# Kernel optimization log

Hardware: AMD Instinct MI355X
Metric: run time of the kernel (lower is better)

The kernel has to match this reference:

```python
import math
import jax, jax.numpy as jnp
import numpy as np

HEADS = 16
DIM_HEAD = 64
BSZ = 16        # block_size
EPS = 1e-8


def _flip_every_two(t):
    # t: (B, nblk, z, d) -> flip adjacent pairs along nblk
    B, nblk = t.shape[0], t.shape[1]
    t = t.reshape(B, nblk // 2, 2, *t.shape[2:])
    t = jnp.flip(t, axis=2)
    return t.reshape(B, nblk, *t.shape[3:])


def setup_inputs() -> dict:
    key = jax.random.key(0)
    k1, k2, k3 = jax.random.split(key, 3)
    b, n, dim = 4, 8192, 1024
    inner = HEADS * DIM_HEAD
    x = jax.random.normal(k1, (b, n, dim), dtype=jnp.float32)
    w_qkv = jax.random.normal(k2, (dim, inner * 3), dtype=jnp.float32) * 0.02
    w_out = jax.random.normal(k3, (inner, dim), dtype=jnp.float32) * 0.02
    b_out = jnp.zeros((dim,), dtype=jnp.float32)
    return {"x": x, "w_qkv": w_qkv, "w_out": w_out, "b_out": b_out}


def _hattention(x, w_qkv, w_out, b_out):
    b, n, dim = x.shape  # n assumed power of 2 -> no padding needed
    scale = DIM_HEAD ** -0.5

    qkv = x @ w_qkv                                   # (b, n, 3*inner)
    q, k, v = jnp.split(qkv, 3, axis=-1)

    def to_heads(t):
        return t.reshape(b, n, HEADS, DIM_HEAD).transpose(0, 2, 1, 3).reshape(b * HEADS, n, DIM_HEAD)

    q, k, v = map(to_heads, (q, k, v))
    q = q * scale

    num_levels = int(math.log2(n // BSZ)) - 1

    # build coarsened pyramid: q,k averaged over pairs, v summed
    qkvs = [(q, k, v)]
    for _ in range(num_levels):
        B, m, d = q.shape
        q = q.reshape(B, m // 2, 2, d).mean(axis=2)
        k = k.reshape(B, m // 2, 2, d).mean(axis=2)
        v = v.reshape(B, m // 2, 2, d).sum(axis=2)
        qkvs.append((q, k, v))

    def to_blocks(t):
        return t.reshape(t.shape[0], -1, BSZ, DIM_HEAD)

    Ys = []
    L = len(qkvs)
    for ind, (ql, kl, vl) in enumerate(reversed(qkvs)):
        is_last = ind == L - 1
        qb, kb, vb = map(to_blocks, (ql, kl, vl))
        if not is_last:
            kb = _flip_every_two(kb)
            vb = _flip_every_two(vb)
        # block-local unnormalized softmax attention
        S = jnp.einsum('bnid,bnjd->bnij', qb, kb)
        S = S - jnp.max(S, axis=-1, keepdims=True)
        A = jnp.exp(S)
        y = jnp.einsum('bnij,bnjd->bnid', A, vb)
        Asum = A.sum(axis=-1)
        Ys.append((y.reshape(y.shape[0], -1, DIM_HEAD),
                   Asum.reshape(Asum.shape[0], -1)))

    # combine coarse-to-fine by upsampling (repeat by 2) and summing
    Y, A = Ys[0]
    for Yl, Al in Ys[1:]:
        Y = jnp.repeat(Y, 2, axis=1) + Yl
        A = jnp.repeat(A, 2, axis=1) + Al

    out = Y / (A + EPS)[..., None]                    # (b*h, n, d)
    out = out.reshape(b, HEADS, n, DIM_HEAD).transpose(0, 2, 1, 3).reshape(b, n, HEADS * DIM_HEAD)
    return out @ w_out + b_out


def reference(x, w_qkv, w_out, b_out):
    return _hattention(x, w_qkv, w_out, b_out)
```

## Files before the change

### kernel.cpp

```cpp
#include <hip/hip_runtime.h>
#include <hip/hip_bf16.h>

typedef __bf16 bf16_t;
typedef bf16_t bf16x8 __attribute__((ext_vector_type(8)));
typedef float f32x4 __attribute__((ext_vector_type(4)));

#define PROWS 16352

__device__ __forceinline__ void gl_lds16(const bf16_t* g, bf16_t* l) {
  __builtin_amdgcn_global_load_lds(
      (const __attribute__((address_space(1))) void*)g,
      (__attribute__((address_space(3))) void*)l,
      16, 0, 0);
}

__device__ __forceinline__ void load8f(const bf16_t* p, float* f) {
  bf16x8 v = *(const bf16x8*)p;
#pragma unroll
  for (int e = 0; e < 8; ++e) f[e] = (float)v[e];
}
__device__ __forceinline__ void store8f(bf16_t* p, const float* f) {
  bf16x8 v;
#pragma unroll
  for (int e = 0; e < 8; ++e) v[e] = (bf16_t)f[e];
  *(bf16x8*)p = v;
}

__global__ __launch_bounds__(256) void cvt_f32_to_bf16(const float* __restrict__ in,
                                                       bf16_t* __restrict__ o) {
  size_t gid = (size_t)blockIdx.x * 256 + threadIdx.x;
  const float4* p = (const float4*)in + gid * 2;
  float4 a = p[0], b = p[1];
  bf16x8 v;
  v[0] = (bf16_t)a.x; v[1] = (bf16_t)a.y; v[2] = (bf16_t)a.z; v[3] = (bf16_t)a.w;
  v[4] = (bf16_t)b.x; v[5] = (bf16_t)b.y; v[6] = (bf16_t)b.z; v[7] = (bf16_t)b.w;
  *(bf16x8*)(o + gid * 8) = v;
}

__global__ __launch_bounds__(256) void transpose_to_bf16(const float* __restrict__ w,
                                                         bf16_t* __restrict__ wT,
                                                         int K, int N) {
  __shared__ float t[32][33];
  int bx = blockIdx.x, by = blockIdx.y;
  int tx = threadIdx.x & 31, ty = threadIdx.x >> 5;
#pragma unroll
  for (int r = ty; r < 32; r += 8)
    t[r][tx] = w[(size_t)(by * 32 + r) * N + bx * 32 + tx];
  __syncthreads();
#pragma unroll
  for (int r = ty; r < 32; r += 8)
    wT[(size_t)(bx * 32 + r) * K + by * 32 + tx] = (bf16_t)t[tx][r];
}

template <int EPI>
__global__ __launch_bounds__(512, 2) void gemm256p(const bf16_t* __restrict__ A,
                                                   const bf16_t* __restrict__ Bt,
                                                   float* __restrict__ Cp,
                                                   const float* __restrict__ bias,
                                                   bf16_t* __restrict__ Pq,
                                                   bf16_t* __restrict__ Pk,
                                                   bf16_t* __restrict__ Pv,
                                                   int ldc, int nTilesN, int tilesPerBlock) {
  __shared__ __align__(16) bf16_t As[2 * 256 * 64];
  __shared__ __align__(16) bf16_t Bs[2 * 256 * 64];
  const int LD = 1024;
  const int tid = threadIdx.x;
  const int w = tid >> 6, lane = tid & 63;

  const int chunk = (blockIdx.x & 7) * 32 + (blockIdx.x >> 3);
  const int tile0 = chunk * tilesPerBlock;
  const int nSteps = tilesPerBlock * 16;

  const int wr = w >> 2, wc = w & 3;
  const int lr = lane & 15, lg = lane >> 4;
  const int sw = lr & 7;
  f32x4 acc[8][4] = {};

  auto stageHalf = [&](const bf16_t* __restrict__ G, int rbase, int kt,
                       bf16_t* lbuf, int h) {
#pragma unroll
    for (int j = 0; j < 2; ++j) {
      int b = j * 8 + w;
      int r3 = lane >> 3;
      int k8 = (lane & 7) ^ r3;
      gl_lds16(G + (size_t)(rbase + h * 128 + b * 8 + r3) * LD + kt + k8 * 8,
               lbuf + h * 8192 + b * 512);
    }
  };

  int ntEc = tile0 % nTilesN;
  int bmE = (tile0 / nTilesN) * 256, bnE = ntEc * 256;
  int nt2c = ntEc, bm2 = bmE, bn2 = bnE, kt2 = 128;

  stageHalf(Bt, bnE, 0, Bs, 0); stageHalf(Bt, bnE, 0, Bs, 1);
  stageHalf(A, bmE, 0, As, 0);  stageHalf(A, bmE, 0, As, 1);
  stageHalf(Bt, bnE, 64, Bs + 16384, 0); stageHalf(Bt, bnE, 64, Bs + 16384, 1);
  stageHalf(A, bmE, 64, As + 16384, 0);  stageHalf(A, bmE, 64, As + 16384, 1);
  asm volatile("s_waitcnt vmcnt(8)" ::: "memory");
  __syncthreads();

  for (int g = 0; g < nSteps; ++g) {
    const int c = g & 1;
    bf16_t* Abuf = As + c * 16384;
    bf16_t* Bbuf = Bs + c * 16384;
    const bool pf = (g + 2) < nSteps;
    bf16x8 bfrag[4][2];

#pragma unroll
    for (int p = 0; p < 4; ++p) {
      bf16x8 afrag[2][2];
#pragma unroll
      for (int fi = 0; fi < 2; ++fi)
#pragma unroll
        for (int kk = 0; kk < 2; ++kk)
          afrag[fi][kk] = *(const bf16x8*)&Abuf[(wr * 128 + p * 32 + fi * 16 + lr) * 64 +
                                                (((kk * 4 + lg) ^ sw) * 8)];
      if (p == 0) {
#pragma unroll
        for (int fj = 0; fj < 4; ++fj)
#pragma unroll
          for (int kk = 0; kk < 2; ++kk)
            bfrag[fj][kk] = *(const bf16x8*)&Bbuf[(wc * 64 + fj * 16 + lr) * 64 +
                                                  (((kk * 4 + lg) ^ sw) * 8)];
      }
      if (pf) {
        if (p == 1) stageHalf(Bt, bn2, kt2, Bbuf, 0);
        if (p == 2) stageHalf(Bt, bn2, kt2, Bbuf, 1);
        if (p == 3) { stageHalf(A, bm2, kt2, Abuf, 0); stageHalf(A, bm2, kt2, Abuf, 1); }
      }
      __builtin_amdgcn_s_barrier();
      asm volatile("s_waitcnt lgkmcnt(0)" ::: "memory");
      __builtin_amdgcn_sched_barrier(0);
      __builtin_amdgcn_s_setprio(1);
#pragma unroll
      for (int kk = 0; kk < 2; ++kk)
#pragma unroll
        for (int fi = 0; fi < 2; ++fi)
#pragma unroll
          for (int fj = 0; fj < 4; ++fj)
            acc[p * 2 + fi][fj] = __builtin_amdgcn_mfma_f32_16x16x32_bf16(
                afrag[fi][kk], bfrag[fj][kk], acc[p * 2 + fi][fj], 0, 0, 0);
      __builtin_amdgcn_s_setprio(0);
      if (p == 3) {
        if (pf) asm volatile("s_waitcnt vmcnt(8)" ::: "memory");
        else    asm volatile("s_waitcnt vmcnt(0)" ::: "memory");
      }
      __builtin_amdgcn_s_barrier();
    }

    kt2 += 64;
    if (kt2 == 1024) {
      kt2 = 0; ++nt2c; bn2 += 256;
      if (nt2c == nTilesN) { nt2c = 0; bn2 = 0; bm2 += 256; }
    }

    if ((g & 15) == 15) {
      if (EPI == 1) {
        float bv[4];
#pragma unroll
        for (int fj = 0; fj < 4; ++fj) bv[fj] = bias[bnE + wc * 64 + fj * 16 + lr];
#pragma unroll
        for (int fi = 0; fi < 8; ++fi)
#pragma unroll
          for (int fj = 0; fj < 4; ++fj)
#pragma unroll
            for (int r = 0; r < 4; ++r) {
              int row = bmE + wr * 128 + fi * 16 + lg * 4 + r;
              int col = bnE + wc * 64 + fj * 16 + lr;
              Cp[(size_t)row * ldc + col] = acc[fi][fj][r] + bv[fj];
            }
      } else {
        const int trow0 = (bmE & 8191) + wr * 128 + lg * 4;
        const int hgRow = (bmE >> 13) << 4;
#pragma unroll
        for (int fj = 0; fj < 4; ++fj) {
          int col = bnE + wc * 64 + fj * 16 + lr;
          int tns = col >> 10, col10 = col & 1023;
          int h = col10 >> 6, d = col10 & 63;
          bf16_t* Pt = (tns == 0) ? Pq : (tns == 1 ? Pk : Pv);
          bf16_t* bp = Pt + ((size_t)(hgRow + h) * PROWS + trow0) * 64 + d;
          float scl = (tns == 0) ? 0.125f : 1.f;
#pragma unroll
          for (int fi = 0; fi < 8; ++fi)
#pragma unroll
            for (int r = 0; r < 4; ++r)
              bp[(fi * 16 + r) * 64] = (bf16_t)(acc[fi][fj][r] * scl);
        }
      }
#pragma unroll
      for (int fi = 0; fi < 8; ++fi)
#pragma unroll
        for (int fj = 0; fj < 4; ++fj) acc[fi][fj] = (f32x4){};
      ++ntEc; bnE += 256;
      if (ntEc == nTilesN) { ntEc = 0; bnE = 0; bmE += 256; }
    }
  }
}

__global__ __launch_bounds__(512) void coarsen_tree(bf16_t* __restrict__ Pq,
                                                    bf16_t* __restrict__ Pk,
                                                    bf16_t* __restrict__ Pv) {
  __shared__ float l6s[8][64];
  const int poffA[9] = {0, 8192, 12288, 14336, 15360, 15872, 16128, 16256, 16320};
  const int hg = blockIdx.x >> 4, win = blockIdx.x & 15;
  const int tid = threadIdx.x;
  const int d8 = tid & 7;
  const int tb = tid >> 3;
  const int wv = tid >> 6;
  const size_t base = (size_t)hg * PROWS;
  const int r0 = win * 512 + tb * 8;

#pragma unroll 1
  for (int tensor = 0; tensor < 3; ++tensor) {
    bf16_t* P = (tensor == 0) ? Pq : (tensor == 1 ? Pk : Pv);
    const float sc = (tensor == 2) ? 1.f : 0.5f;
    float v[8][8];
#pragma unroll
    for (int i = 0; i < 8; ++i) load8f(P + (base + r0 + i) * 64 + d8 * 8, v[i]);
    float a1[4][8];
#pragma unroll
    for (int i = 0; i < 4; ++i) {
#pragma unroll
      for (int e = 0; e < 8; ++e) a1[i][e] = sc * (v[2 * i][e] + v[2 * i + 1][e]);
      store8f(P + (base + poffA[1] + win * 256 + tb * 4 + i) * 64 + d8 * 8, a1[i]);
    }
    float a2[2][8];
#pragma unroll
    for (int i = 0; i < 2; ++i) {
#pragma unroll
      for (int e = 0; e < 8; ++e) a2[i][e] = sc * (a1[2 * i][e] + a1[2 * i + 1][e]);
      store8f(P + (base + poffA[2] + win * 128 + tb * 2 + i) * 64 + d8 * 8, a2[i]);
    }
    float a3[8];
#pragma unroll
    for (int e = 0; e < 8; ++e) a3[e] = sc * (a2[0][e] + a2[1][e]);
    store8f(P + (base + poffA[3] + win * 64 + tb) * 64 + d8 * 8, a3);
    float a4[8];
#pragma unroll
    for (int e = 0; e < 8; ++e) a4[e] = sc * (a3[e] + __shfl_xor(a3[e], 8, 64));
    if ((tb & 1) == 0) store8f(P + (base + poffA[4] + win * 32 + (tb >> 1)) * 64 + d8 * 8, a4);
    float a5[8];
#pragma unroll
    for (int e = 0; e < 8; ++e) a5[e] = sc * (a4[e] + __shfl_xor(a4[e], 16, 64));
    if ((tb & 3) == 0) store8f(P + (base + poffA[5] + win * 16 + (tb >> 2)) * 64 + d8 * 8, a5);
    float a6[8];
#pragma unroll
    for (int e = 0; e < 8; ++e) a6[e] = sc * (a5[e] + __shfl_xor(a5[e], 32, 64));
    if ((tb & 7) == 0) {
      bf16x8 o;
#pragma unroll
      for (int e = 0; e < 8; ++e) { l6s[wv][d8 * 8 + e] = a6[e]; o[e] = (bf16_t)a6[e]; }
      *(bf16x8*)(P + (base + poffA[6] + win * 8 + wv) * 64 + d8 * 8) = o;
    }
    __syncthreads();
    if (tid < 32) {
      int pr = tid >> 3;
      float a7[8];
#pragma unroll
      for (int e = 0; e < 8; ++e)
        a7[e] = sc * (l6s[2 * pr][d8 * 8 + e] + l6s[2 * pr + 1][d8 * 8 + e]);
      store8f(P + (base + poffA[7] + win * 4 + pr) * 64 + d8 * 8, a7);
      if (pr < 2) {
        float a8[8];
#pragma unroll
        for (int e = 0; e < 8; ++e)
          a8[e] = sc * (sc * (l6s[4 * pr][d8 * 8 + e] + l6s[4 * pr + 1][d8 * 8 + e]) +
                        sc * (l6s[4 * pr + 2][d8 * 8 + e] + l6s[4 * pr + 3][d8 * 8 + e]));
        store8f(P + (base + poffA[8] + win * 2 + pr) * 64 + d8 * 8, a8);
      }
    }
    __syncthreads();
  }
}


__global__ __launch_bounds__(256) void attn_hi(bf16_t* __restrict__ Pq,
                                               const bf16_t* __restrict__ Pk,
                                               const bf16_t* __restrict__ Pv,
                                               float* __restrict__ Asum) {
  const int poffA[9] = {0, 8192, 12288, 14336, 15360, 15872, 16128, 16256, 16320};
  const int tid = threadIdx.x;
  const int wv = tid >> 6, lane = tid & 63;
  const int lr = lane & 15, lg = lane >> 4;

  int bid = blockIdx.x * 4 + wv;
  int l = 4, cnt = 2048;
  while (bid >= cnt) { bid -= cnt; cnt >>= 1; ++l; }
  const int lg2nblk = 9 - l;
  const int blk = bid & ((1 << lg2nblk) - 1);
  const int hg = bid >> lg2nblk;
  const int kvblk = blk ^ 1;
  const size_t qbase = (size_t)hg * PROWS + poffA[l] + blk * 16;
  const size_t kvbase = (size_t)hg * PROWS + poffA[l] + kvblk * 16;

  f32x4 s = {};
#pragma unroll
  for (int c = 0; c < 2; ++c) {
    bf16x8 ak = *(const bf16x8*)(Pk + (kvbase + lr) * 64 + c * 32 + lg * 8);
    bf16x8 bq = *(const bf16x8*)(Pq + (qbase + lr) * 64 + c * 32 + lg * 8);
    s = __builtin_amdgcn_mfma_f32_16x16x32_bf16(ak, bq, s, 0, 0, 0);
  }
  float mx = fmaxf(fmaxf(s[0], s[1]), fmaxf(s[2], s[3]));
  mx = fmaxf(mx, __shfl_xor(mx, 16, 64));
  mx = fmaxf(mx, __shfl_xor(mx, 32, 64));
  float a[4]; float asum = 0.f;
#pragma unroll
  for (int r = 0; r < 4; ++r) { a[r] = (float)(bf16_t)__expf(s[r] - mx); asum += a[r]; }
  asum += __shfl_xor(asum, 16, 64);
  asum += __shfl_xor(asum, 32, 64);
  if (lg == 0) Asum[qbase + lr] = asum;

  const int src0 = (2 * lg) * 16 + lr;
  const int src1 = (2 * lg + 1) * 16 + lr;
  bf16x8 pa;
#pragma unroll
  for (int r = 0; r < 4; ++r) {
    float c0 = __shfl(a[r], src0, 64);
    float c1 = __shfl(a[r], src1, 64);
    pa[r]     = (lg < 2) ? (bf16_t)c0 : (bf16_t)0.f;
    pa[r + 4] = (lg < 2) ? (bf16_t)c1 : (bf16_t)0.f;
  }
#pragma unroll
  for (int dt = 0; dt < 4; ++dt) {
    bf16x8 vf;
    if (lg < 2) {
#pragma unroll
      for (int e = 0; e < 8; ++e) vf[e] = Pv[(kvbase + lg * 8 + e) * 64 + dt * 16 + lr];
    } else {
#pragma unroll
      for (int e = 0; e < 8; ++e) vf[e] = (bf16_t)0.f;
    }
    f32x4 y = __builtin_amdgcn_mfma_f32_16x16x32_bf16(pa, vf, (f32x4){}, 0, 0, 0);
#pragma unroll
    for (int r = 0; r < 4; ++r)
      Pq[(qbase + 4 * lg + r) * 64 + dt * 16 + lr] = (bf16_t)y[r];
  }
}

__global__ __launch_bounds__(256) void attn_comb(const bf16_t* __restrict__ Pq,
                                                 const bf16_t* __restrict__ Pk,
                                                 const bf16_t* __restrict__ Pv,
                                                 const float* __restrict__ Ab,
                                                 bf16_t* __restrict__ attnb) {
  __shared__ __align__(16) bf16_t yl[480 * 72];
  __shared__ float asl[480];
  const int poffA[9] = {0, 8192, 12288, 14336, 15360, 15872, 16128, 16256, 16320};
  const int loffA[4] = {0, 256, 384, 448};
  const int hg = blockIdx.x >> 5, win = blockIdx.x & 31;
  const int tid = threadIdx.x;
  const int wv = tid >> 6, lane = tid & 63;
  const int lr = lane & 15, lg = lane >> 4;

  auto do_attn = [&](int l, int blkL) {
    const int nb = 16 >> l;
    const int blk = win * nb + blkL;
    const int kvblk = l ? (blk ^ 1) : blk;
    const size_t qbase = (size_t)hg * PROWS + poffA[l] + (size_t)blk * 16;
    const size_t kvbase = (size_t)hg * PROWS + poffA[l] + (size_t)kvblk * 16;
    const int lrow = loffA[l] + blkL * 16;

    f32x4 s = {};
#pragma unroll
    for (int c = 0; c < 2; ++c) {
      bf16x8 ak = *(const bf16x8*)(Pk + (kvbase + lr) * 64 + c * 32 + lg * 8);
      bf16x8 bq = *(const bf16x8*)(Pq + (qbase + lr) * 64 + c * 32 + lg * 8);
      s = __builtin_amdgcn_mfma_f32_16x16x32_bf16(ak, bq, s, 0, 0, 0);
    }
    float mx = fmaxf(fmaxf(s[0], s[1]), fmaxf(s[2], s[3]));
    mx = fmaxf(mx, __shfl_xor(mx, 16, 64));
    mx = fmaxf(mx, __shfl_xor(mx, 32, 64));
    float a[4]; float asum = 0.f;
#pragma unroll
    for (int r = 0; r < 4; ++r) { a[r] = (float)(bf16_t)__expf(s[r] - mx); asum += a[r]; }
    asum += __shfl_xor(asum, 16, 64);
    asum += __shfl_xor(asum, 32, 64);
    if (lg == 0) asl[lrow + lr] = asum;

    const int src0 = (2 * lg) * 16 + lr;
    const int src1 = (2 * lg + 1) * 16 + lr;
    bf16x8 pa;
#pragma unroll
    for (int r = 0; r < 4; ++r) {
      float c0 = __shfl(a[r], src0, 64);
      float c1 = __shfl(a[r], src1, 64);
      pa[r]     = (lg < 2) ? (bf16_t)c0 : (bf16_t)0.f;
      pa[r + 4] = (lg < 2) ? (bf16_t)c1 : (bf16_t)0.f;
    }
#pragma unroll
    for (int dt = 0; dt < 4; ++dt) {
      bf16x8 vf;
      if (lg < 2) {
#pragma unroll
        for (int e = 0; e < 8; ++e) vf[e] = Pv[(kvbase + lg * 8 + e) * 64 + dt * 16 + lr];
      } else {
#pragma unroll
        for (int e = 0; e < 8; ++e) vf[e] = (bf16_t)0.f;
      }
      f32x4 y = __builtin_amdgcn_mfma_f32_16x16x32_bf16(pa, vf, (f32x4){}, 0, 0, 0);
#pragma unroll
      for (int r = 0; r < 4; ++r)
        yl[(lrow + 4 * lg + r) * 72 + dt * 16 + lr] = (bf16_t)y[r];
    }
  };

  do_attn(0, wv * 4 + 0); do_attn(0, wv * 4 + 1);
  do_attn(0, wv * 4 + 2); do_attn(0, wv * 4 + 3);
  do_attn(1, wv * 2 + 0); do_attn(1, wv * 2 + 1);
  do_attn(2, wv);
  if (wv < 2) do_attn(3, wv);
  __syncthreads();

  const int d8 = tid & 7, rg = tid >> 3;
#pragma unroll
  for (int i = 0; i < 8; ++i) {
    const int r = rg * 8 + i;
    const int t = win * 256 + r;
    float acc[8] = {};
    float asum = 0.f;
#pragma unroll
    for (int l = 0; l < 4; ++l) {
      const int row = loffA[l] + (r >> l);
      asum += asl[row];
      bf16x8 v = *(const bf16x8*)&yl[row * 72 + d8 * 8];
#pragma unroll
      for (int e = 0; e < 8; ++e) acc[e] += (float)v[e];
    }
#pragma unroll
    for (int l = 4; l < 9; ++l) {
      const size_t grow = (size_t)hg * PROWS + poffA[l] + (t >> l);
      asum += Ab[grow];
      bf16x8 v = *(const bf16x8*)(Pq + grow * 64 + d8 * 8);
#pragma unroll
      for (int e = 0; e < 8; ++e) acc[e] += (float)v[e];
    }
    const float inv = 1.f / (asum + 1e-8f);
    bf16x8 o;
#pragma unroll
    for (int e = 0; e < 8; ++e) o[e] = (bf16_t)(acc[e] * inv);
    *(bf16x8*)(attnb + ((size_t)(hg >> 4) * 8192 + t) * 1024 + (hg & 15) * 64 + d8 * 8) = o;
  }
}

extern "C" void kernel_launch(void* const* d_in, const int* in_sizes, int n_in,
                              void* d_out, int out_size, void* d_ws, size_t ws_size,
                              hipStream_t stream) {
  const float* x = (const float*)d_in[0];
  const float* wqkv = (const float*)d_in[1];
  const float* wout = (const float*)d_in[2];
  const float* bout = (const float*)d_in[3];
  float* out = (float*)d_out;
  (void)in_sizes; (void)n_in; (void)out_size; (void)ws_size;

  char* base = (char*)d_ws;
  bf16_t* Pq    = (bf16_t*)(base + 0);
  bf16_t* Pk    = (bf16_t*)(base + 133955584);
  bf16_t* Pv    = (bf16_t*)(base + 267911168);
  float*  Ab    = (float*)(base + 401866752);
  bf16_t* woutT = (bf16_t*)(base + 406052864);
  bf16_t* x_bf  = (bf16_t*)(base + 408150016);
  bf16_t* wqkvT = (bf16_t*)(base + 475258880);
  bf16_t* attnb = (bf16_t*)(base + 408150016);

  cvt_f32_to_bf16<<<16384, 256, 0, stream>>>(x, x_bf);
  transpose_to_bf16<<<dim3(96, 32), 256, 0, stream>>>(wqkv, wqkvT, 1024, 3072);
  transpose_to_bf16<<<dim3(32, 32), 256, 0, stream>>>(wout, woutT, 1024, 1024);

  gemm256p<0><<<256, 512, 0, stream>>>(x_bf, wqkvT, nullptr, nullptr, Pq, Pk, Pv,
                                       3072, 12, 6);

  coarsen_tree<<<1024, 512, 0, stream>>>(Pq, Pk, Pv);

  attn_hi<<<992, 256, 0, stream>>>(Pq, Pk, Pv, Ab);
  attn_comb<<<2048, 256, 0, stream>>>(Pq, Pk, Pv, Ab, attnb);

  gemm256p<1><<<256, 512, 0, stream>>>(attnb, woutT, out, bout, nullptr, nullptr, nullptr,
                                       1024, 4, 2);
}
```

Baseline: 592.7 us.

## Skip storing pyramid levels 1-3; recompute coarse q/k/v on the fly in attn_comb

The coarsening kernel no longer writes levels 1-3 of the q/k/v pyramid. It sums 8 rows directly and emits only levels 4-8, with finer-grained blocks (256 threads, 2048 blocks). attn_comb recomputes coarse q and k for levels 1-3 by averaging 2^l fine rows on the fly. It handles coarse v by spreading the attention weights across the fine rows and running several MFMA chunks. This removes a large amount of global writes and reads of intermediate levels, in exchange for more loads and MFMAs in attn_comb and slightly different bf16 rounding of the coarse levels.

```diff
diff --git a/kernel.cpp b/kernel.cpp
--- a/kernel.cpp
+++ b/kernel.cpp
@@ -197,82 +197,73 @@
   }
 }
 
-__global__ __launch_bounds__(512) void coarsen_tree(bf16_t* __restrict__ Pq,
+__global__ __launch_bounds__(256) void coarsen_lite(bf16_t* __restrict__ Pq,
                                                     bf16_t* __restrict__ Pk,
                                                     bf16_t* __restrict__ Pv) {
-  __shared__ float l6s[8][64];
+  __shared__ float l6s[4][64];
   const int poffA[9] = {0, 8192, 12288, 14336, 15360, 15872, 16128, 16256, 16320};
-  const int hg = blockIdx.x >> 4, win = blockIdx.x & 15;
+  const int hg = blockIdx.x >> 5, win = blockIdx.x & 31;
   const int tid = threadIdx.x;
-  const int d8 = tid & 7;
-  const int tb = tid >> 3;
-  const int wv = tid >> 6;
+  const int d8 = tid & 7, tb = tid >> 3, wv = tid >> 6;
   const size_t base = (size_t)hg * PROWS;
-  const int r0 = win * 512 + tb * 8;
+  const int r0 = win * 256 + tb * 8;
 
 #pragma unroll 1
   for (int tensor = 0; tensor < 3; ++tensor) {
     bf16_t* P = (tensor == 0) ? Pq : (tensor == 1 ? Pk : Pv);
-    const float sc = (tensor == 2) ? 1.f : 0.5f;
-    float v[8][8];
-#pragma unroll
-    for (int i = 0; i < 8; ++i) load8f(P + (base + r0 + i) * 64 + d8 * 8, v[i]);
-    float a1[4][8];
-#pragma unroll
-    for (int i = 0; i < 4; ++i) {
-#pragma unroll
-      for (int e = 0; e < 8; ++e) a1[i][e] = sc * (v[2 * i][e] + v[2 * i + 1][e]);
-      store8f(P + (base + poffA[1] + win * 256 + tb * 4 + i) * 64 + d8 * 8, a1[i]);
-    }
-    float a2[2][8];
-#pragma unroll
-    for (int i = 0; i < 2; ++i) {
-#pragma unroll
-      for (int e = 0; e < 8; ++e) a2[i][e] = sc * (a1[2 * i][e] + a1[2 * i + 1][e]);
-      store8f(P + (base + poffA[2] + win * 128 + tb * 2 + i) * 64 + d8 * 8, a2[i]);
-    }
-    float a3[8];
-#pragma unroll
-    for (int e = 0; e < 8; ++e) a3[e] = sc * (a2[0][e] + a2[1][e]);
-    store8f(P + (base + poffA[3] + win * 64 + tb) * 64 + d8 * 8, a3);
-    float a4[8];
-#pragma unroll
-    for (int e = 0; e < 8; ++e) a4[e] = sc * (a3[e] + __shfl_xor(a3[e], 8, 64));
-    if ((tb & 1) == 0) store8f(P + (base + poffA[4] + win * 32 + (tb >> 1)) * 64 + d8 * 8, a4);
-    float a5[8];
-#pragma unroll
-    for (int e = 0; e < 8; ++e) a5[e] = sc * (a4[e] + __shfl_xor(a4[e], 16, 64));
-    if ((tb & 3) == 0) store8f(P + (base + poffA[5] + win * 16 + (tb >> 2)) * 64 + d8 * 8, a5);
-    float a6[8];
-#pragma unroll
-    for (int e = 0; e < 8; ++e) a6[e] = sc * (a5[e] + __shfl_xor(a5[e], 32, 64));
+    const bool isv = (tensor == 2);
+    float s3[8] = {}, t[8], o[8];
+#pragma unroll
+    for (int i = 0; i < 8; ++i) {
+      load8f(P + (base + r0 + i) * 64 + d8 * 8, t);
+#pragma unroll
+      for (int e = 0; e < 8; ++e) s3[e] += t[e];
+    }
+    float s4[8], s5[8], s6[8];
+#pragma unroll
+    for (int e = 0; e < 8; ++e) s4[e] = s3[e] + __shfl_xor(s3[e], 8, 64);
+    if ((tb & 1) == 0) {
+      float sc = isv ? 1.f : 0.0625f;
+#pragma unroll
+      for (int e = 0; e < 8; ++e) o[e] = s4[e] * sc;
+      store8f(P + (base + poffA[4] + win * 16 + (tb >> 1)) * 64 + d8 * 8, o);
+    }
+#pragma unroll
+    for (int e = 0; e < 8; ++e) s5[e] = s4[e] + __shfl_xor(s4[e], 16, 64);
+    if ((tb & 3) == 0) {
+      float sc = isv ? 1.f : 0.03125f;
+#pragma unroll
+      for (int e = 0; e < 8; ++e) o[e] = s5[e] * sc;
+      store8f(P + (base + poffA[5] + win * 8 + (tb >> 2)) * 64 + d8 * 8, o);
+    }
+#pragma unroll
+    for (int e = 0; e < 8; ++e) s6[e] = s5[e] + __shfl_xor(s5[e], 32, 64);
     if ((tb & 7) == 0) {
-      bf16x8 o;
-#pragma unroll
-      for (int e = 0; e < 8; ++e) { l6s[wv][d8 * 8 + e] = a6[e]; o[e] = (bf16_t)a6[e]; }
-      *(bf16x8*)(P + (base + poffA[6] + win * 8 + wv) * 64 + d8 * 8) = o;
+      float sc = isv ? 1.f : 0.015625f;
+#pragma unroll
+      for (int e = 0; e < 8; ++e) { o[e] = s6[e] * sc; l6s[wv][d8 * 8 + e] = s6[e]; }
+      store8f(P + (base + poffA[6] + win * 4 + wv) * 64 + d8 * 8, o);
     }
     __syncthreads();
-    if (tid < 32) {
-      int pr = tid >> 3;
-      float a7[8];
+    if (tid < 16) {
+      int pr = tid >> 3, dd = tid & 7;
+      float sc7 = isv ? 1.f : 0.0078125f;
 #pragma unroll
       for (int e = 0; e < 8; ++e)
-        a7[e] = sc * (l6s[2 * pr][d8 * 8 + e] + l6s[2 * pr + 1][d8 * 8 + e]);
-      store8f(P + (base + poffA[7] + win * 4 + pr) * 64 + d8 * 8, a7);
-      if (pr < 2) {
-        float a8[8];
-#pragma unroll
-        for (int e = 0; e < 8; ++e)
-          a8[e] = sc * (sc * (l6s[4 * pr][d8 * 8 + e] + l6s[4 * pr + 1][d8 * 8 + e]) +
-                        sc * (l6s[4 * pr + 2][d8 * 8 + e] + l6s[4 * pr + 3][d8 * 8 + e]));
-        store8f(P + (base + poffA[8] + win * 2 + pr) * 64 + d8 * 8, a8);
-      }
+        o[e] = (l6s[2 * pr][dd * 8 + e] + l6s[2 * pr + 1][dd * 8 + e]) * sc7;
+      store8f(P + (base + poffA[7] + win * 2 + pr) * 64 + dd * 8, o);
+    }
+    if (tid < 8) {
+      float sc8 = isv ? 1.f : 0.00390625f;
+#pragma unroll
+      for (int e = 0; e < 8; ++e)
+        o[e] = (l6s[0][d8 * 8 + e] + l6s[1][d8 * 8 + e] +
+                l6s[2][d8 * 8 + e] + l6s[3][d8 * 8 + e]) * sc8;
+      store8f(P + (base + poffA[8] + win) * 64 + d8 * 8, o);
     }
     __syncthreads();
   }
 }
-
 
 __global__ __launch_bounds__(256) void attn_hi(bf16_t* __restrict__ Pq,
                                                const bf16_t* __restrict__ Pk,
@@ -350,22 +341,38 @@
   const int tid = threadIdx.x;
   const int wv = tid >> 6, lane = tid & 63;
   const int lr = lane & 15, lg = lane >> 4;
+  const size_t hb = (size_t)hg * PROWS;
 
   auto do_attn = [&](int l, int blkL) {
-    const int nb = 16 >> l;
-    const int blk = win * nb + blkL;
+    const int blk = win * (16 >> l) + blkL;
     const int kvblk = l ? (blk ^ 1) : blk;
-    const size_t qbase = (size_t)hg * PROWS + poffA[l] + (size_t)blk * 16;
-    const size_t kvbase = (size_t)hg * PROWS + poffA[l] + (size_t)kvblk * 16;
     const int lrow = loffA[l] + blkL * 16;
+    const int q0 = (blk * 16 + lr) << l;
+    const int k0 = (kvblk * 16 + lr) << l;
+    const int kv0 = (kvblk * 16) << l;
+    const float scl = 1.f / (float)(1 << l);
 
     f32x4 s = {};
 #pragma unroll
     for (int c = 0; c < 2; ++c) {
-      bf16x8 ak = *(const bf16x8*)(Pk + (kvbase + lr) * 64 + c * 32 + lg * 8);
-      bf16x8 bq = *(const bf16x8*)(Pq + (qbase + lr) * 64 + c * 32 + lg * 8);
+      float fk[8] = {}, fq[8] = {}, t[8];
+      for (int m = 0; m < (1 << l); ++m) {
+        load8f(Pk + (hb + k0 + m) * 64 + c * 32 + lg * 8, t);
+#pragma unroll
+        for (int e = 0; e < 8; ++e) fk[e] += t[e];
+        load8f(Pq + (hb + q0 + m) * 64 + c * 32 + lg * 8, t);
+#pragma unroll
+        for (int e = 0; e < 8; ++e) fq[e] += t[e];
+      }
+      bf16x8 ak, bq;
+#pragma unroll
+      for (int e = 0; e < 8; ++e) {
+        ak[e] = (bf16_t)(fk[e] * scl);
+        bq[e] = (bf16_t)(fq[e] * scl);
+      }
       s = __builtin_amdgcn_mfma_f32_16x16x32_bf16(ak, bq, s, 0, 0, 0);
     }
+
     float mx = fmaxf(fmaxf(s[0], s[1]), fmaxf(s[2], s[3]));
     mx = fmaxf(mx, __shfl_xor(mx, 16, 64));
     mx = fmaxf(mx, __shfl_xor(mx, 32, 64));
@@ -376,30 +383,72 @@
     asum += __shfl_xor(asum, 32, 64);
     if (lg == 0) asl[lrow + lr] = asum;
 
-    const int src0 = (2 * lg) * 16 + lr;
-    const int src1 = (2 * lg + 1) * 16 + lr;
-    bf16x8 pa;
-#pragma unroll
-    for (int r = 0; r < 4; ++r) {
-      float c0 = __shfl(a[r], src0, 64);
-      float c1 = __shfl(a[r], src1, 64);
-      pa[r]     = (lg < 2) ? (bf16_t)c0 : (bf16_t)0.f;
-      pa[r + 4] = (lg < 2) ? (bf16_t)c1 : (bf16_t)0.f;
-    }
-#pragma unroll
-    for (int dt = 0; dt < 4; ++dt) {
-      bf16x8 vf;
-      if (lg < 2) {
-#pragma unroll
-        for (int e = 0; e < 8; ++e) vf[e] = Pv[(kvbase + lg * 8 + e) * 64 + dt * 16 + lr];
-      } else {
-#pragma unroll
-        for (int e = 0; e < 8; ++e) vf[e] = (bf16_t)0.f;
-      }
-      f32x4 y = __builtin_amdgcn_mfma_f32_16x16x32_bf16(pa, vf, (f32x4){}, 0, 0, 0);
-#pragma unroll
-      for (int r = 0; r < 4; ++r)
-        yl[(lrow + 4 * lg + r) * 72 + dt * 16 + lr] = (bf16_t)y[r];
+    if (l == 0) {
+      const int src0 = (2 * lg) * 16 + lr;
+      const int src1 = (2 * lg + 1) * 16 + lr;
+      bf16x8 pa;
+#pragma unroll
+      for (int r = 0; r < 4; ++r) {
+        float c0 = __shfl(a[r], src0, 64);
+        float c1 = __shfl(a[r], src1, 64);
+        pa[r]     = (lg < 2) ? (bf16_t)c0 : (bf16_t)0.f;
+        pa[r + 4] = (lg < 2) ? (bf16_t)c1 : (bf16_t)0.f;
+      }
+#pragma unroll
+      for (int dt = 0; dt < 4; ++dt) {
+        bf16x8 vf;
+        if (lg < 2) {
+#pragma unroll
+          for (int e = 0; e < 8; ++e) vf[e] = Pv[(hb + kv0 + lg * 8 + e) * 64 + dt * 16 + lr];
+        } else {
+#pragma unroll
+          for (int e = 0; e < 8; ++e) vf[e] = (bf16_t)0.f;
+        }
+        f32x4 y = __builtin_amdgcn_mfma_f32_16x16x32_bf16(pa, vf, (f32x4){}, 0, 0, 0);
+#pragma unroll
+        for (int r = 0; r < 4; ++r)
+          yl[(lrow + 4 * lg + r) * 72 + dt * 16 + lr] = (bf16_t)y[r];
+      }
+    } else {
+      const int nch = 1 << (l - 1);
+      bf16x8 pa[4];
+      for (int ch = 0; ch < nch; ++ch) {
+        if (l == 1) {
+#pragma unroll
+          for (int e = 0; e < 8; ++e) pa[ch][e] = (bf16_t)a[e >> 1];
+        } else if (l == 2) {
+          int src = (2 * ch + (lg >> 1)) * 16 + lr;
+          float t0 = __shfl(a[0], src, 64), t1 = __shfl(a[1], src, 64);
+          float t2 = __shfl(a[2], src, 64), t3 = __shfl(a[3], src, 64);
+          float vlo = (lg & 1) ? t2 : t0;
+          float vhi = (lg & 1) ? t3 : t1;
+#pragma unroll
+          for (int e = 0; e < 4; ++e) { pa[ch][e] = (bf16_t)vlo; pa[ch][e + 4] = (bf16_t)vhi; }
+        } else {
+          int src = ch * 16 + lr;
+          float t0 = __shfl(a[0], src, 64), t1 = __shfl(a[1], src, 64);
+          float t2 = __shfl(a[2], src, 64), t3 = __shfl(a[3], src, 64);
+          float v01 = (lg & 1) ? t1 : t0;
+          float v23 = (lg & 1) ? t3 : t2;
+          float vv = (lg & 2) ? v23 : v01;
+#pragma unroll
+          for (int e = 0; e < 8; ++e) pa[ch][e] = (bf16_t)vv;
+        }
+      }
+#pragma unroll
+      for (int dt = 0; dt < 4; ++dt) {
+        f32x4 y = {};
+        for (int ch = 0; ch < nch; ++ch) {
+          bf16x8 vf;
+#pragma unroll
+          for (int e = 0; e < 8; ++e)
+            vf[e] = Pv[(hb + kv0 + ch * 32 + lg * 8 + e) * 64 + dt * 16 + lr];
+          y = __builtin_amdgcn_mfma_f32_16x16x32_bf16(pa[ch], vf, y, 0, 0, 0);
+        }
+#pragma unroll
+        for (int r = 0; r < 4; ++r)
+          yl[(lrow + 4 * lg + r) * 72 + dt * 16 + lr] = (bf16_t)y[r];
+      }
     }
   };
 
@@ -427,7 +476,7 @@
     }
 #pragma unroll
     for (int l = 4; l < 9; ++l) {
-      const size_t grow = (size_t)hg * PROWS + poffA[l] + (t >> l);
+      const size_t grow = hb + poffA[l] + (t >> l);
       asum += Ab[grow];
       bf16x8 v = *(const bf16x8*)(Pq + grow * 64 + d8 * 8);
 #pragma unroll
@@ -468,7 +517,7 @@
   gemm256p<0><<<256, 512, 0, stream>>>(x_bf, wqkvT, nullptr, nullptr, Pq, Pk, Pv,
                                        3072, 12, 6);
 
-  coarsen_tree<<<1024, 512, 0, stream>>>(Pq, Pk, Pv);
+  coarsen_lite<<<2048, 256, 0, stream>>>(Pq, Pk, Pv);
 
   attn_hi<<<992, 256, 0, stream>>>(Pq, Pk, Pv, Ab);
   attn_comb<<<2048, 256, 0, stream>>>(Pq, Pk, Pv, Ab, attnb);
```

Result: faster. 550.1 us (-7.2%).
